# Kernel tuning notes

Measured on AMD Instinct MI355X. Metric: run time of the kernel, lower is better.

The kernel has to match this reference:

```python
import jax, jax.numpy as jnp
import numpy as np

B, CIN, COUT, H, W = 2, 64, 64, 64, 2048
EPS = 1e-5


def unfold3(x):
    # x: [B, C, H, W] -> [B, H*W, 9, C], torch.nn.Unfold(k=3, pad=1) layout
    b, c, h, w = x.shape
    xp = jnp.pad(x, ((0, 0), (0, 0), (1, 1), (1, 1)))
    # kernel positions in row-major (ki, kj) order; index 4 is the center
    patches = jnp.stack([xp[:, :, i:i + h, j:j + w]
                         for i in range(3) for j in range(3)], axis=2)  # [B,C,9,H,W]
    return patches.reshape(b, c, 9, h * w).transpose(0, 3, 2, 1)  # [B,HW,9,C]


def setup_inputs() -> dict:
    key = jax.random.key(0)
    ks = jax.random.split(key, 8)
    x = jax.random.normal(ks[0], (B, 3 + CIN, H, W), dtype=jnp.float32)
    mask = jax.random.randint(ks[1], (B, 1, H, W), 0, 2, dtype=jnp.int32)
    w_spatial = jax.random.normal(ks[2], (CIN, 4), dtype=jnp.float32) * 0.5
    b_spatial = jax.random.normal(ks[3], (CIN,), dtype=jnp.float32) * 0.1
    w_channel = jax.random.normal(ks[4], (CIN, 4), dtype=jnp.float32) * 0.5
    b_channel = jax.random.normal(ks[5], (CIN,), dtype=jnp.float32) * 0.1
    w_agg = jax.random.normal(ks[6], (COUT, 9 * CIN), dtype=jnp.float32) * (1.0 / np.sqrt(9 * CIN))
    gamma = jnp.ones((COUT,), dtype=jnp.float32)
    beta = jnp.zeros((COUT,), dtype=jnp.float32)
    return {"x": x, "mask": mask, "w_spatial": w_spatial, "b_spatial": b_spatial,
            "w_channel": w_channel, "b_channel": b_channel, "w_agg": w_agg,
            "gamma": gamma, "beta": beta}


def reference(x, mask, w_spatial, b_spatial, w_channel, b_channel, w_agg, gamma, beta):
    b, _, h, w = x.shape
    x_un = unfold3(x)                              # [B,HW,9,3+C]
    feat = x_un[..., 3:]                           # [B,HW,9,C]
    x_pn = x_un[..., :3]                           # [B,HW,9,3]
    m_un = unfold3(mask.astype(jnp.float32))       # [B,HW,9,1]

    rng = jnp.linalg.norm(x_pn, axis=-1, keepdims=True)
    x_pn4 = jnp.concatenate([x_pn, rng], axis=-1)  # [B,HW,9,4]
    pn_p0 = x_pn4 - x_pn4[:, :, 4:5, :]            # relative to 3x3 center

    ws = jnp.einsum('bnkm,cm->bnkc', pn_p0, w_spatial) + b_spatial
    wc = jnp.einsum('bnkm,cm->bnkc', pn_p0, w_channel) + b_channel
    ws = jnp.max(ws, axis=3, keepdims=True)        # [B,HW,9,1]
    wc = jnp.max(wc, axis=2, keepdims=True)        # [B,HW,1,C]
    ws = jax.nn.softmax(ws, axis=2)
    wc = jax.nn.softmax(wc, axis=3)
    weights = (ws + wc) * m_un                     # [B,HW,9,C]

    feat = (weights * feat).reshape(b, h * w, 9 * CIN)
    out = jnp.einsum('bnf,of->bno', feat, w_agg)   # [B,HW,COUT]
    out = out.transpose(0, 2, 1)                   # [B,COUT,HW]

    # BatchNorm1d in training mode: stats over (batch, spatial) per channel
    mu = jnp.mean(out, axis=(0, 2), keepdims=True)
    var = jnp.mean((out - mu) ** 2, axis=(0, 2), keepdims=True)
    out = (out - mu) * jax.lax.rsqrt(var + EPS)
    out = out * gamma[None, :, None] + beta[None, :, None]
    out = jax.nn.relu(out)
    return out.reshape(b, COUT, h, w)              # Fold(k=1) == reshape
```

## Files before the change

kernel.cpp:

```cpp
#include <hip/hip_runtime.h>
#include <hip/hip_bf16.h>
#include <math.h>
#include <cstddef>

#define HDIM 64
#define WDIM 2048
#define HW   (HDIM*WDIM)
#define BATCH 2
#define CIN  64
#define COUT 64
#define XC   (3+CIN)
#define NPIX (BATCH*HW)
#define NBLK (NPIX/64)
#define NB2  (NBLK*2)
#define EPS  1e-5f

typedef short  short8  __attribute__((ext_vector_type(8)));
typedef float  f32x16  __attribute__((ext_vector_type(16)));

__device__ __forceinline__ unsigned short f2bf(float f) {
    unsigned int u = __float_as_uint(f);
    u += 0x7fff + ((u >> 16) & 1);
    return (unsigned short)(u >> 16);
}

struct __align__(16) SmemA {
    float wsm[9][64];
    float mk[9][64];
    float winv[64];
    float wc[64][64];
    union {
        unsigned short V[64][72];
        float wspart[9][4][64];
    } u;
};

__global__ __launch_bounds__(256)
void kernelW(const float* __restrict__ w_agg, unsigned short* __restrict__ wbf)
{
    int t = blockIdx.x*256 + threadIdx.x;
    int co  = t / 72;
    int rem = t % 72;
    int kk  = rem >> 3;
    int ks  = (rem >> 1) & 3;
    int half= rem & 1;
    const float* src = w_agg + (size_t)co*576 + kk*64 + ks*16 + half*8;
    unsigned long long pk0 = 0, pk1 = 0;
    #pragma unroll
    for (int j=0;j<4;++j) pk0 |= (unsigned long long)f2bf(src[j])   << (16*j);
    #pragma unroll
    for (int j=0;j<4;++j) pk1 |= (unsigned long long)f2bf(src[4+j]) << (16*j);
    unsigned long long* dst =
        (unsigned long long*)(wbf + ((size_t)(((kk*4+ks)*2+half)*64 + co))*8);
    dst[0] = pk0; dst[1] = pk1;
}

__global__ __launch_bounds__(256, 4)
void kernelA(const float* __restrict__ x, const int* __restrict__ mask,
             const float* __restrict__ w_sp, const float* __restrict__ b_sp,
             const float* __restrict__ w_ch, const float* __restrict__ b_ch,
             const unsigned short* __restrict__ wbf,
             float* __restrict__ out, float* __restrict__ psum, float* __restrict__ psq)
{
    __shared__ SmemA s;
    const int tid = threadIdx.x;
    const int bid = blockIdx.x;
    const int b  = bid >> 11;
    const int r  = bid & 2047;
    const int h  = r >> 5;
    const int w0 = (r & 31) << 6;

    const int px = tid & 63;
    const int q  = tid >> 6;

    float p[9][4];
    float mkr[9];
    {
        const int wpix = w0 + px;
        #pragma unroll
        for (int k = 0; k < 9; ++k) {
            int hh = h + k/3 - 1;
            int ww = wpix + k%3 - 1;
            bool in = (hh >= 0) && (hh < HDIM) && (ww >= 0) && (ww < WDIM);
            float p0=0.f, p1=0.f, p2=0.f, mv=0.f;
            if (in) {
                size_t base = ((size_t)(b*XC)*HDIM + hh)*(size_t)WDIM + ww;
                p0 = x[base];
                p1 = x[base + (size_t)HW];
                p2 = x[base + 2*(size_t)HW];
                mv = (float)mask[((size_t)b*HDIM + hh)*(size_t)WDIM + ww];
            }
            p[k][0]=p0; p[k][1]=p1; p[k][2]=p2;
            p[k][3]=sqrtf(p0*p0 + p1*p1 + p2*p2);
            mkr[k]=mv;
        }
        float c0=p[4][0], c1=p[4][1], c2=p[4][2], c3=p[4][3];
        #pragma unroll
        for (int k = 0; k < 9; ++k) {
            p[k][0]-=c0; p[k][1]-=c1; p[k][2]-=c2; p[k][3]-=c3;
        }
    }

    float wsp[9];
    #pragma unroll
    for (int k=0;k<9;++k) wsp[k] = -1e30f;
    for (int cc = 0; cc < 16; ++cc) {
        int c = q*16 + cc;
        float a0=w_sp[c*4+0], a1=w_sp[c*4+1], a2=w_sp[c*4+2], a3=w_sp[c*4+3], bs=b_sp[c];
        float d0=w_ch[c*4+0], d1=w_ch[c*4+1], d2=w_ch[c*4+2], d3=w_ch[c*4+3], bc=b_ch[c];
        float tmax = bc;
        wsp[4] = fmaxf(wsp[4], bs);
        #pragma unroll
        for (int k=0;k<9;++k) {
            if (k == 4) continue;
            float sv = fmaf(p[k][0],a0, fmaf(p[k][1],a1, fmaf(p[k][2],a2, fmaf(p[k][3],a3, bs))));
            wsp[k] = fmaxf(wsp[k], sv);
            float tv = fmaf(p[k][0],d0, fmaf(p[k][1],d1, fmaf(p[k][2],d2, fmaf(p[k][3],d3, bc))));
            tmax = fmaxf(tmax, tv);
        }
        s.wc[c][px] = tmax;
    }
    #pragma unroll
    for (int k=0;k<9;++k) s.u.wspart[k][q][px] = wsp[k];
    __syncthreads();

    if (q == 0) {
        float v[9]; float mx = -1e30f;
        #pragma unroll
        for (int k=0;k<9;++k) {
            float a = s.u.wspart[k][0][px];
            a = fmaxf(a, s.u.wspart[k][1][px]);
            a = fmaxf(a, s.u.wspart[k][2][px]);
            a = fmaxf(a, s.u.wspart[k][3][px]);
            v[k]=a; mx=fmaxf(mx,a);
        }
        float sum=0.f;
        #pragma unroll
        for (int k=0;k<9;++k) { v[k]=__expf(v[k]-mx); sum+=v[k]; }
        float inv = 1.0f/sum;
        #pragma unroll
        for (int k=0;k<9;++k) {
            s.wsm[k][px] = v[k]*inv*mkr[k];
            s.mk[k][px]  = mkr[k];
        }
    } else if (q == 1) {
        float mx=-1e30f;
        for (int c=0;c<64;++c) mx = fmaxf(mx, s.wc[c][px]);
        float sum=0.f;
        for (int c=0;c<64;++c) {
            float e = __expf(s.wc[c][px]-mx);
            s.wc[c][px] = e;
            sum += e;
        }
        s.winv[px] = 1.0f/sum;
    }
    __syncthreads();

    const int lane = tid & 63;
    const int wv   = tid >> 6;
    const int mrow = lane & 31;
    const int half = lane >> 5;
    const int co0  = (wv & 1) * 32;
    const int px0  = (wv >> 1) * 32;

    const short8* aswz = (const short8*)wbf;

    f32x16 acc;
    #pragma unroll
    for (int i=0;i<16;++i) acc[i]=0.f;

    for (int kk = 0; kk < 9; ++kk) {
        short8 af[4];
        #pragma unroll
        for (int ks=0; ks<4; ++ks)
            af[ks] = aswz[(size_t)(((kk*4+ks)*2+half)*64) + co0 + mrow];

        {
            int di = kk/3 - 1, dj = (kk%3) - 1;
            int hh = h + di;
            int ww = w0 + px + dj;
            bool inb = (hh>=0) && (hh<HDIM) && (ww>=0) && (ww<WDIM);
            int hhc = hh<0?0:(hh>HDIM-1?HDIM-1:hh);
            int wwc = ww<0?0:(ww>WDIM-1?WDIM-1:ww);
            const float* xb = x + ((size_t)(b*XC + 3)*HDIM + hhc)*(size_t)WDIM + wwc;
            float a_k = s.wsm[kk][px];
            float m2  = s.mk[kk][px] * s.winv[px];
            unsigned int packed[8];
            #pragma unroll
            for (int j=0;j<8;++j) {
                unsigned c0 = 16u*q + 2u*j;
                float f0 = inb ? xb[(size_t)c0*HW]       : 0.f;
                float f1 = inb ? xb[(size_t)(c0+1)*HW]   : 0.f;
                float w0f = fmaf(m2, s.wc[c0][px],   a_k) * f0;
                float w1f = fmaf(m2, s.wc[c0+1][px], a_k) * f1;
                __hip_bfloat162 h2 = __float22bfloat162_rn(float2{w0f, w1f});
                unsigned int u; __builtin_memcpy(&u, &h2, 4);
                packed[j] = u;
            }
            uint4* vp = (uint4*)&s.u.V[px][16*q];
            vp[0] = uint4{packed[0],packed[1],packed[2],packed[3]};
            vp[1] = uint4{packed[4],packed[5],packed[6],packed[7]};
        }
        __syncthreads();
        #pragma unroll
        for (int ks=0; ks<4; ++ks) {
            short8 bf = *(const short8*)&s.u.V[px0+mrow][ks*16 + half*8];
            acc = __builtin_amdgcn_mfma_f32_32x32x16_bf16(af[ks], bf, acc, 0, 0, 0);
        }
        __syncthreads();
    }

    const int pxg = w0 + px0 + mrow;
    #pragma unroll
    for (int reg=0; reg<16; ++reg) {
        int row = (reg&3) + 8*(reg>>2) + 4*half;
        int co  = co0 + row;
        float v = acc[reg];
        out[((size_t)(b*COUT+co))*HW + (size_t)h*WDIM + pxg] = v;
        float s1 = v, s2 = v*v;
        #pragma unroll
        for (int m=1; m<32; m<<=1) {
            s1 += __shfl_xor(s1, m, 64);
            s2 += __shfl_xor(s2, m, 64);
        }
        if (mrow == 0) {
            psum[(size_t)co*NB2 + bid*2 + (wv>>1)] = s1;
            psq [(size_t)co*NB2 + bid*2 + (wv>>1)] = s2;
        }
    }
}

__global__ __launch_bounds__(256)
void kernelB(const float* __restrict__ psum, const float* __restrict__ psq,
             float* __restrict__ stats)
{
    int co = blockIdx.x;
    int tid = threadIdx.x;
    float s=0.f, sq=0.f;
    for (int j = tid; j < NB2; j += 256) {
        s  += psum[(size_t)co*NB2 + j];
        sq += psq [(size_t)co*NB2 + j];
    }
    #pragma unroll
    for (int m=1; m<64; m<<=1) { s += __shfl_xor(s,m,64); sq += __shfl_xor(sq,m,64); }
    __shared__ float rs[4], rq[4];
    int wv = tid>>6;
    if ((tid&63)==0){ rs[wv]=s; rq[wv]=sq; }
    __syncthreads();
    if (tid==0) {
        float S = rs[0]+rs[1]+rs[2]+rs[3];
        float Q = rq[0]+rq[1]+rq[2]+rq[3];
        float mu = S / (float)NPIX;
        float var = Q/(float)NPIX - mu*mu;
        stats[co]      = mu;
        stats[64+co]   = rsqrtf(var + EPS);
    }
}

__global__ __launch_bounds__(256)
void kernelC(float* __restrict__ out, const float* __restrict__ stats,
             const float* __restrict__ gamma, const float* __restrict__ beta)
{
    size_t idx8 = (size_t)blockIdx.x*256 + threadIdx.x;
    size_t flat = idx8*8;
    int co = (int)((flat >> 17) & 63);
    float mu = stats[co], rstd = stats[64+co];
    float g  = gamma[co]*rstd;
    float bb = fmaf(-mu, g, beta[co]);
    #pragma unroll
    for (int t=0;t<2;++t) {
        float4 v = *(float4*)(out + flat + t*4);
        v.x = fmaxf(fmaf(v.x, g, bb), 0.f);
        v.y = fmaxf(fmaf(v.y, g, bb), 0.f);
        v.z = fmaxf(fmaf(v.z, g, bb), 0.f);
        v.w = fmaxf(fmaf(v.w, g, bb), 0.f);
        *(float4*)(out + flat + t*4) = v;
    }
}

extern "C" void kernel_launch(void* const* d_in, const int* in_sizes, int n_in,
                              void* d_out, int out_size, void* d_ws, size_t ws_size,
                              hipStream_t stream)
{
    const float* x     = (const float*)d_in[0];
    const int*   mask  = (const int*)  d_in[1];
    const float* w_sp  = (const float*)d_in[2];
    const float* b_sp  = (const float*)d_in[3];
    const float* w_ch  = (const float*)d_in[4];
    const float* b_ch  = (const float*)d_in[5];
    const float* w_agg = (const float*)d_in[6];
    const float* gamma = (const float*)d_in[7];
    const float* beta  = (const float*)d_in[8];
    float* out  = (float*)d_out;
    float* psum = (float*)d_ws;
    float* psq  = psum + (size_t)COUT*NB2;
    float* stats= psq  + (size_t)COUT*NB2;
    unsigned short* wbf = (unsigned short*)(stats + 128);

    kernelW<<<18, 256, 0, stream>>>(w_agg, wbf);
    kernelA<<<NBLK, 256, 0, stream>>>(x, mask, w_sp, b_sp, w_ch, b_ch, wbf, out, psum, psq);
    kernelB<<<COUT, 256, 0, stream>>>(psum, psq, stats);
    int grid_c = (NPIX*COUT/8)/256;
    kernelC<<<grid_c, 256, 0, stream>>>(out, stats, gamma, beta);
}
```

Baseline: 263.6 us.

## Double-buffer feature staging and parallelize channel softmax across all quads

Splits the per-pixel channel softmax so all four thread groups each compute exp over their 16 channels, with partial maxima and sums exchanged through shared memory, instead of a single group doing all 64 serially. The main 9-tap loop now uses a double-buffered V tile: global loads for the next tap are issued before the current MFMAs, and the weighted bf16 pack is written to the other buffer afterward. This removes one barrier per iteration and overlaps global latency with MFMA work, at the cost of more LDS and 16 extra live registers per thread.

New measurement: 290.3 us. +10.1%, slower.

```diff
diff --git a/kernel.cpp b/kernel.cpp
--- a/kernel.cpp
+++ b/kernel.cpp
@@ -26,11 +26,11 @@
 
 struct __align__(16) SmemA {
     float wsm[9][64];
-    float mk[9][64];
-    float winv[64];
+    float wcpart[4][64];
+    float wcsum[4][64];
     float wc[64][64];
     union {
-        unsigned short V[64][72];
+        unsigned short V[2][64][72];
         float wspart[9][4][64];
     } u;
 };
@@ -104,6 +104,8 @@
     float wsp[9];
     #pragma unroll
     for (int k=0;k<9;++k) wsp[k] = -1e30f;
+    float tmaxv[16];
+    float cqm = -1e30f;
     for (int cc = 0; cc < 16; ++cc) {
         int c = q*16 + cc;
         float a0=w_sp[c*4+0], a1=w_sp[c*4+1], a2=w_sp[c*4+2], a3=w_sp[c*4+3], bs=b_sp[c];
@@ -118,12 +120,26 @@
             float tv = fmaf(p[k][0],d0, fmaf(p[k][1],d1, fmaf(p[k][2],d2, fmaf(p[k][3],d3, bc))));
             tmax = fmaxf(tmax, tv);
         }
-        s.wc[c][px] = tmax;
+        tmaxv[cc] = tmax;
+        cqm = fmaxf(cqm, tmax);
     }
     #pragma unroll
     for (int k=0;k<9;++k) s.u.wspart[k][q][px] = wsp[k];
+    s.wcpart[q][px] = cqm;
     __syncthreads();
 
+    {
+        float mxc = fmaxf(fmaxf(s.wcpart[0][px], s.wcpart[1][px]),
+                          fmaxf(s.wcpart[2][px], s.wcpart[3][px]));
+        float sum = 0.f;
+        #pragma unroll
+        for (int cc=0; cc<16; ++cc) {
+            float e = __expf(tmaxv[cc] - mxc);
+            s.wc[q*16+cc][px] = e;
+            sum += e;
+        }
+        s.wcsum[q][px] = sum;
+    }
     if (q == 0) {
         float v[9]; float mx = -1e30f;
         #pragma unroll
@@ -139,22 +155,12 @@
         for (int k=0;k<9;++k) { v[k]=__expf(v[k]-mx); sum+=v[k]; }
         float inv = 1.0f/sum;
         #pragma unroll
-        for (int k=0;k<9;++k) {
-            s.wsm[k][px] = v[k]*inv*mkr[k];
-            s.mk[k][px]  = mkr[k];
-        }
-    } else if (q == 1) {
-        float mx=-1e30f;
-        for (int c=0;c<64;++c) mx = fmaxf(mx, s.wc[c][px]);
-        float sum=0.f;
-        for (int c=0;c<64;++c) {
-            float e = __expf(s.wc[c][px]-mx);
-            s.wc[c][px] = e;
-            sum += e;
-        }
-        s.winv[px] = 1.0f/sum;
+        for (int k=0;k<9;++k) s.wsm[k][px] = v[k]*inv*mkr[k];
     }
     __syncthreads();
+
+    const float winv = 1.0f / (s.wcsum[0][px] + s.wcsum[1][px] +
+                               s.wcsum[2][px] + s.wcsum[3][px]);
 
     const int lane = tid & 63;
     const int wv   = tid >> 6;
@@ -169,45 +175,63 @@
     #pragma unroll
     for (int i=0;i<16;++i) acc[i]=0.f;
 
+    auto stage_load = [&](int kk, float* f) {
+        int di = kk/3 - 1, dj = (kk%3) - 1;
+        int hh = h + di;
+        int ww = w0 + px + dj;
+        bool inb = (hh>=0) && (hh<HDIM) && (ww>=0) && (ww<WDIM);
+        int hhc = hh<0?0:(hh>HDIM-1?HDIM-1:hh);
+        int wwc = ww<0?0:(ww>WDIM-1?WDIM-1:ww);
+        const float* xb = x + ((size_t)(b*XC + 3)*HDIM + hhc)*(size_t)WDIM + wwc;
+        #pragma unroll
+        for (int j=0;j<16;++j)
+            f[j] = inb ? xb[(size_t)(16*q + j)*HW] : 0.f;
+    };
+    auto stage_write = [&](int kk, const float* f, int buf) {
+        float a_k = s.wsm[kk][px];
+        float m2  = mkr[kk] * winv;
+        unsigned int packed[8];
+        #pragma unroll
+        for (int j=0;j<8;++j) {
+            unsigned c0 = 16u*q + 2u*j;
+            float w0f = fmaf(m2, s.wc[c0][px],   a_k) * f[2*j];
+            float w1f = fmaf(m2, s.wc[c0+1][px], a_k) * f[2*j+1];
+            __hip_bfloat162 h2 = __float22bfloat162_rn(float2{w0f, w1f});
+            unsigned int u; __builtin_memcpy(&u, &h2, 4);
+            packed[j] = u;
+        }
+        uint4* vp = (uint4*)&s.u.V[buf][px][16*q];
+        vp[0] = uint4{packed[0],packed[1],packed[2],packed[3]};
+        vp[1] = uint4{packed[4],packed[5],packed[6],packed[7]};
+    };
+
+    {
+        float f0[16];
+        stage_load(0, f0);
+        stage_write(0, f0, 0);
+        __syncthreads();
+    }
+
     for (int kk = 0; kk < 9; ++kk) {
-        short8 af[4];
+        short8 afc[4];
         #pragma unroll
         for (int ks=0; ks<4; ++ks)
-            af[ks] = aswz[(size_t)(((kk*4+ks)*2+half)*64) + co0 + mrow];
-
-        {
-            int di = kk/3 - 1, dj = (kk%3) - 1;
-            int hh = h + di;
-            int ww = w0 + px + dj;
-            bool inb = (hh>=0) && (hh<HDIM) && (ww>=0) && (ww<WDIM);
-            int hhc = hh<0?0:(hh>HDIM-1?HDIM-1:hh);
-            int wwc = ww<0?0:(ww>WDIM-1?WDIM-1:ww);
-            const float* xb = x + ((size_t)(b*XC + 3)*HDIM + hhc)*(size_t)WDIM + wwc;
-            float a_k = s.wsm[kk][px];
-            float m2  = s.mk[kk][px] * s.winv[px];
-            unsigned int packed[8];
-            #pragma unroll
-            for (int j=0;j<8;++j) {
-                unsigned c0 = 16u*q + 2u*j;
-                float f0 = inb ? xb[(size_t)c0*HW]       : 0.f;
-                float f1 = inb ? xb[(size_t)(c0+1)*HW]   : 0.f;
-                float w0f = fmaf(m2, s.wc[c0][px],   a_k) * f0;
-                float w1f = fmaf(m2, s.wc[c0+1][px], a_k) * f1;
-                __hip_bfloat162 h2 = __float22bfloat162_rn(float2{w0f, w1f});
-                unsigned int u; __builtin_memcpy(&u, &h2, 4);
-                packed[j] = u;
-            }
-            uint4* vp = (uint4*)&s.u.V[px][16*q];
-            vp[0] = uint4{packed[0],packed[1],packed[2],packed[3]};
-            vp[1] = uint4{packed[4],packed[5],packed[6],packed[7]};
-        }
-        __syncthreads();
+            afc[ks] = aswz[(size_t)(((kk*4+ks)*2+half)*64) + co0 + mrow];
+
+        float fn[16];
+        if (kk < 8) stage_load(kk+1, fn);
+
+        const unsigned short* Vb = &s.u.V[kk & 1][px0 + mrow][0];
         #pragma unroll
         for (int ks=0; ks<4; ++ks) {
-            short8 bf = *(const short8*)&s.u.V[px0+mrow][ks*16 + half*8];
-            acc = __builtin_amdgcn_mfma_f32_32x32x16_bf16(af[ks], bf, acc, 0, 0, 0);
-        }
-        __syncthreads();
+            short8 bf = *(const short8*)&Vb[ks*16 + half*8];
+            acc = __builtin_amdgcn_mfma_f32_32x32x16_bf16(afc[ks], bf, acc, 0, 0, 0);
+        }
+
+        if (kk < 8) {
+            stage_write(kk+1, fn, (kk & 1) ^ 1);
+            __syncthreads();
+        }
     }
 
     const int pxg = w0 + px0 + mrow;
```

## Parallelize channel softmax across all waves and pack weights as bf16 in LDS

Applied to the files above, without the earlier changes.

The channel-softmax max and sum are now computed cooperatively by all four waves, each over its 16 channels with partial max/sum exchanged through shared memory, instead of one wave doing a serial 64-channel pass. The exponentials are stored as packed bf16 pairs, which halves that shared-memory array. The mask array is read from registers instead of LDS. The smaller LDS footprint allows raising the launch-bounds occupancy hint from 4 to 6 blocks; the cost is bf16 rounding of the softmax numerators and possible register pressure from the extra logits kept per thread.

Result: slower. 516.0 us (+95.8%).

```diff
diff --git a/kernel.cpp b/kernel.cpp
--- a/kernel.cpp
+++ b/kernel.cpp
@@ -26,9 +26,9 @@
 
 struct __align__(16) SmemA {
     float wsm[9][64];
-    float mk[9][64];
-    float winv[64];
-    float wc[64][64];
+    float wcpart[4][64];
+    float wcsum[4][64];
+    unsigned int wcp[32][64];
     union {
         unsigned short V[64][72];
         float wspart[9][4][64];
@@ -55,7 +55,7 @@
     dst[0] = pk0; dst[1] = pk1;
 }
 
-__global__ __launch_bounds__(256, 4)
+__global__ __launch_bounds__(256, 6)
 void kernelA(const float* __restrict__ x, const int* __restrict__ mask,
              const float* __restrict__ w_sp, const float* __restrict__ b_sp,
              const float* __restrict__ w_ch, const float* __restrict__ b_ch,
@@ -104,6 +104,8 @@
     float wsp[9];
     #pragma unroll
     for (int k=0;k<9;++k) wsp[k] = -1e30f;
+    float wclog[16];
+    float cqm = -1e30f;
     for (int cc = 0; cc < 16; ++cc) {
         int c = q*16 + cc;
         float a0=w_sp[c*4+0], a1=w_sp[c*4+1], a2=w_sp[c*4+2], a3=w_sp[c*4+3], bs=b_sp[c];
@@ -118,12 +120,28 @@
             float tv = fmaf(p[k][0],d0, fmaf(p[k][1],d1, fmaf(p[k][2],d2, fmaf(p[k][3],d3, bc))));
             tmax = fmaxf(tmax, tv);
         }
-        s.wc[c][px] = tmax;
+        wclog[cc] = tmax;
+        cqm = fmaxf(cqm, tmax);
     }
     #pragma unroll
     for (int k=0;k<9;++k) s.u.wspart[k][q][px] = wsp[k];
+    s.wcpart[q][px] = cqm;
     __syncthreads();
 
+    {
+        float M = fmaxf(fmaxf(s.wcpart[0][px], s.wcpart[1][px]),
+                        fmaxf(s.wcpart[2][px], s.wcpart[3][px]));
+        float sum = 0.f;
+        #pragma unroll
+        for (int j=0; j<8; ++j) {
+            float e0 = __expf(wclog[2*j]   - M);
+            float e1 = __expf(wclog[2*j+1] - M);
+            sum += e0 + e1;
+            unsigned int u = (unsigned int)f2bf(e0) | ((unsigned int)f2bf(e1) << 16);
+            s.wcp[q*8+j][px] = u;
+        }
+        s.wcsum[q][px] = sum;
+    }
     if (q == 0) {
         float v[9]; float mx = -1e30f;
         #pragma unroll
@@ -139,22 +157,12 @@
         for (int k=0;k<9;++k) { v[k]=__expf(v[k]-mx); sum+=v[k]; }
         float inv = 1.0f/sum;
         #pragma unroll
-        for (int k=0;k<9;++k) {
-            s.wsm[k][px] = v[k]*inv*mkr[k];
-            s.mk[k][px]  = mkr[k];
-        }
-    } else if (q == 1) {
-        float mx=-1e30f;
-        for (int c=0;c<64;++c) mx = fmaxf(mx, s.wc[c][px]);
-        float sum=0.f;
-        for (int c=0;c<64;++c) {
-            float e = __expf(s.wc[c][px]-mx);
-            s.wc[c][px] = e;
-            sum += e;
-        }
-        s.winv[px] = 1.0f/sum;
+        for (int k=0;k<9;++k) s.wsm[k][px] = v[k]*inv*mkr[k];
     }
     __syncthreads();
+
+    const float winv = 1.0f / (s.wcsum[0][px] + s.wcsum[1][px] +
+                               s.wcsum[2][px] + s.wcsum[3][px]);
 
     const int lane = tid & 63;
     const int wv   = tid >> 6;
@@ -184,15 +192,18 @@
             int wwc = ww<0?0:(ww>WDIM-1?WDIM-1:ww);
             const float* xb = x + ((size_t)(b*XC + 3)*HDIM + hhc)*(size_t)WDIM + wwc;
             float a_k = s.wsm[kk][px];
-            float m2  = s.mk[kk][px] * s.winv[px];
+            float m2  = mkr[kk] * winv;
             unsigned int packed[8];
             #pragma unroll
             for (int j=0;j<8;++j) {
                 unsigned c0 = 16u*q + 2u*j;
+                unsigned int ew = s.wcp[q*8+j][px];
+                float e0 = __uint_as_float(ew << 16);
+                float e1 = __uint_as_float(ew & 0xffff0000u);
                 float f0 = inb ? xb[(size_t)c0*HW]       : 0.f;
                 float f1 = inb ? xb[(size_t)(c0+1)*HW]   : 0.f;
-                float w0f = fmaf(m2, s.wc[c0][px],   a_k) * f0;
-                float w1f = fmaf(m2, s.wc[c0+1][px], a_k) * f1;
+                float w0f = fmaf(m2, e0, a_k) * f0;
+                float w1f = fmaf(m2, e1, a_k) * f1;
                 __hip_bfloat162 h2 = __float22bfloat162_rn(float2{w0f, w1f});
                 unsigned int u; __builtin_memcpy(&u, &h2, 4);
                 packed[j] = u;
```
